# Performance work log

Hardware: AMD Instinct MI355X
Metric: run time of the kernel (lower is better)

Reference implementation:

```python
import jax, jax.numpy as jnp
import numpy as np

N = 100000
E = 1600000
IN_DIM = 256
HID = 256
OUT = 64
K = 10
ALPHA = 0.1


def setup_inputs() -> dict:
    key = jax.random.key(0)
    ks = jax.random.split(key, 8)
    x = jax.random.normal(ks[0], (N, IN_DIM), dtype=jnp.float32)
    edge_index = jax.random.randint(ks[1], (2, E), 0, N, dtype=jnp.int64)
    # Linear params (torch default-ish scale)
    W1 = jax.random.normal(ks[2], (IN_DIM, HID), dtype=jnp.float32) / np.sqrt(IN_DIM)
    b1 = jnp.zeros((HID,), dtype=jnp.float32)
    W2 = jax.random.normal(ks[3], (HID, OUT), dtype=jnp.float32) / np.sqrt(HID)
    b2 = jnp.zeros((OUT,), dtype=jnp.float32)
    alpha = jnp.asarray([ALPHA * (1.0 - ALPHA) ** k for k in range(K + 1)], dtype=jnp.float32)
    return {"x": x, "edge_index": edge_index, "W1": W1, "b1": b1, "W2": W2, "b2": b2, "alpha": alpha}


def reference(x, edge_index, W1, b1, W2, b2, alpha):
    # MLP head (dropout = identity in eval)
    h = jax.nn.relu(x @ W1 + b1) @ W2 + b2  # [N, OUT]

    row, col = edge_index[0], edge_index[1]
    num_nodes = h.shape[0]
    # degree over row (matches torch_geometric degree(row, ...))
    deg = jax.ops.segment_sum(jnp.ones_like(row, dtype=h.dtype), row, num_segments=num_nodes)
    deg_inv_sqrt = jnp.where(deg > 0, jax.lax.rsqrt(jnp.maximum(deg, 1.0)), 0.0)
    norm = deg_inv_sqrt[row] * deg_inv_sqrt[col]  # [E]

    gamma = jax.nn.softmax(alpha)

    def step(carry, g):
        h_cur, acc = carry
        msg = h_cur[col] * norm[:, None]  # gather + scale  [E, OUT]
        h_new = jax.ops.segment_sum(msg, row, num_segments=num_nodes)  # scatter_add
        return (h_new, acc + g * h_new), None

    acc0 = gamma[0] * h
    (_, out), _ = jax.lax.scan(step, (h, acc0), gamma[1:])
    return out
```

## Files before the change

kernel.cpp:

```cpp
#include <hip/hip_runtime.h>
#include <hip/hip_bf16.h>

#define N_NODES 100000
#define N_EDGES 1600000
#define IN_DIM_ 256
#define HID_ 256
#define OUT_ 64
#define KSTEPS 10

typedef __attribute__((ext_vector_type(4))) float f32x4;
typedef __attribute__((ext_vector_type(8))) __bf16 bf16x8;
typedef __attribute__((ext_vector_type(8))) unsigned short u16x8;

static __device__ __forceinline__ unsigned short f2bf(float f) {
    union { float f; unsigned int u; } v; v.f = f;
    unsigned int u = v.u;
    unsigned int r = u + 0x7FFFu + ((u >> 16) & 1u);
    return (unsigned short)(r >> 16);
}
static __device__ __forceinline__ float bflo(unsigned int v) {
    return __uint_as_float(v << 16);
}
static __device__ __forceinline__ float bfhi(unsigned int v) {
    return __uint_as_float(v & 0xFFFF0000u);
}


__global__ void gamma_kernel(const float* __restrict__ alpha, float* __restrict__ gamma) {
    if (threadIdx.x == 0) {
        float m = alpha[0];
        for (int i = 1; i <= KSTEPS; ++i) m = fmaxf(m, alpha[i]);
        float e[KSTEPS + 1];
        float s = 0.f;
        for (int i = 0; i <= KSTEPS; ++i) { e[i] = expf(alpha[i] - m); s += e[i]; }
        float inv = 1.f / s;
        for (int i = 0; i <= KSTEPS; ++i) gamma[i] = e[i] * inv;
    }
}

__global__ void deg_kernel(const int* __restrict__ row, int* __restrict__ deg, int E) {
    int e = blockIdx.x * 256 + threadIdx.x;
    if (e < E) atomicAdd(&deg[row[e]], 1);
}

__global__ void dis_kernel(const int* __restrict__ deg, float* __restrict__ dis, int n) {
    int i = blockIdx.x * 256 + threadIdx.x;
    if (i < n) {
        int d = deg[i];
        dis[i] = d > 0 ? rsqrtf((float)d) : 0.f;
    }
}

__global__ void wcast_kernel(const float* __restrict__ W, unsigned short* __restrict__ wT,
                             int K, int N) {
    int k = blockIdx.x * 256 + threadIdx.x;
    int n = blockIdx.y;
    if (k < K) wT[(size_t)n * K + k] = f2bf(W[(size_t)k * N + n]);
}


__global__ __launch_bounds__(256) void scan_sum_kernel(const int* __restrict__ deg,
                                                       int* __restrict__ bsum, int n) {
    __shared__ int s[256];
    int t = threadIdx.x;
    int i = blockIdx.x * 256 + t;
    s[t] = (i < n) ? deg[i] : 0;
    __syncthreads();
    for (int st = 128; st > 0; st >>= 1) {
        if (t < st) s[t] += s[t + st];
        __syncthreads();
    }
    if (t == 0) bsum[blockIdx.x] = s[0];
}

__global__ __launch_bounds__(512) void scan_block_kernel(int* __restrict__ bsum,
                                                         int* __restrict__ off,
                                                         int nblk, int n) {
    __shared__ int s[512];
    int t = threadIdx.x;
    int v = (t < nblk) ? bsum[t] : 0;
    s[t] = v;
    __syncthreads();
    for (int st = 1; st < 512; st <<= 1) {
        int a = (t >= st) ? s[t - st] : 0;
        __syncthreads();
        s[t] += a;
        __syncthreads();
    }
    if (t < nblk) bsum[t] = s[t] - v;
    if (t == 511) off[n] = s[511];
}

__global__ __launch_bounds__(256) void scan_final_kernel(const int* __restrict__ deg,
                                                         const int* __restrict__ bsum,
                                                         int* __restrict__ off, int n) {
    __shared__ int s[256];
    int t = threadIdx.x;
    int i = blockIdx.x * 256 + t;
    int v = (i < n) ? deg[i] : 0;
    s[t] = v;
    __syncthreads();
    for (int st = 1; st < 256; st <<= 1) {
        int a = (t >= st) ? s[t - st] : 0;
        __syncthreads();
        s[t] += a;
        __syncthreads();
    }
    if (i < n) off[i] = bsum[blockIdx.x] + s[t] - v;
}

__global__ void csr_scatter_kernel(const int* __restrict__ row, const int* __restrict__ col,
                                   const float* __restrict__ dis, const int* __restrict__ off,
                                   int* __restrict__ cursor, int2* __restrict__ ecsr, int E) {
    int e = blockIdx.x * 256 + threadIdx.x;
    if (e < E) {
        int r = row[e], c = col[e];
        float w = dis[r] * dis[c];
        int pos = atomicAdd(&cursor[r], 1);
        int2 p;
        p.x = c;
        p.y = __float_as_int(w);
        ecsr[(size_t)off[r] + pos] = p;
    }
}

__global__ __launch_bounds__(256) void gemm1_kernel(const float* __restrict__ x,
                                                    const unsigned short* __restrict__ w1T,
                                                    const float* __restrict__ b1,
                                                    unsigned short* __restrict__ h1, int M) {
    __shared__ unsigned short As[64][40];
    __shared__ unsigned short Bs[256][40];

    const int tid = threadIdx.x;
    const int lane = tid & 63;
    const int w = tid >> 6;
    const int wr = w >> 1, wc = w & 1;
    const int row0 = blockIdx.x * 64;

    const int am = tid >> 2;
    const int ak = (tid & 3) * 8;

    f32x4 acc[2][8] = {};

    for (int kk = 0; kk < 256; kk += 32) {
        {
            int gr = row0 + am;
            u16x8 av;
            if (gr < M) {
                const float* p = x + (size_t)gr * IN_DIM_ + kk + ak;
                #pragma unroll
                for (int j = 0; j < 8; ++j) av[j] = f2bf(p[j]);
            } else {
                #pragma unroll
                for (int j = 0; j < 8; ++j) av[j] = 0;
            }
            *(u16x8*)&As[am][ak] = av;
        }
        {
            const unsigned short* p = w1T + (size_t)tid * 256 + kk;
            *(u16x8*)&Bs[tid][0]  = *(const u16x8*)&p[0];
            *(u16x8*)&Bs[tid][8]  = *(const u16x8*)&p[8];
            *(u16x8*)&Bs[tid][16] = *(const u16x8*)&p[16];
            *(u16x8*)&Bs[tid][24] = *(const u16x8*)&p[24];
        }
        __syncthreads();

        const int fr = lane & 15;
        const int ko = (lane >> 4) * 8;
        bf16x8 a[2];
        #pragma unroll
        for (int mi = 0; mi < 2; ++mi) a[mi] = *(const bf16x8*)&As[wr * 32 + mi * 16 + fr][ko];
        #pragma unroll
        for (int ni = 0; ni < 8; ++ni) {
            bf16x8 b = *(const bf16x8*)&Bs[wc * 128 + ni * 16 + fr][ko];
            #pragma unroll
            for (int mi = 0; mi < 2; ++mi)
                acc[mi][ni] = __builtin_amdgcn_mfma_f32_16x16x32_bf16(a[mi], b, acc[mi][ni], 0, 0, 0);
        }
        __syncthreads();
    }

    const int fr = lane & 15;
    const int rg = (lane >> 4) * 4;
    #pragma unroll
    for (int mi = 0; mi < 2; ++mi) {
        #pragma unroll
        for (int r = 0; r < 4; ++r) {
            int gm = row0 + wr * 32 + mi * 16 + rg + r;
            if (gm < M) {
                #pragma unroll
                for (int ni = 0; ni < 8; ++ni) {
                    int gn = wc * 128 + ni * 16 + fr;
                    float v = acc[mi][ni][r] + b1[gn];
                    v = fmaxf(v, 0.f);
                    h1[(size_t)gm * HID_ + gn] = f2bf(v);
                }
            }
        }
    }
}

__global__ __launch_bounds__(256) void gemm2_kernel(const unsigned short* __restrict__ h1,
                                                    const unsigned short* __restrict__ w2T,
                                                    const float* __restrict__ b2,
                                                    const float* __restrict__ gamma,
                                                    unsigned short* __restrict__ h,
                                                    float* __restrict__ out, int M) {
    __shared__ unsigned short As[64][40];
    __shared__ unsigned short Bs[64][40];

    const int tid = threadIdx.x;
    const int lane = tid & 63;
    const int w = tid >> 6;
    const int wr = w >> 1, wc = w & 1;
    const int row0 = blockIdx.x * 64;

    const int am = tid >> 2;
    const int ak = (tid & 3) * 8;

    f32x4 acc[2][2] = {};

    for (int kk = 0; kk < 256; kk += 32) {
        {
            int gr = row0 + am;
            if (gr < M) {
                *(u16x8*)&As[am][ak] = *(const u16x8*)&h1[(size_t)gr * HID_ + kk + ak];
            } else {
                u16x8 z = {};
                *(u16x8*)&As[am][ak] = z;
            }
        }
        if (tid < 128) {
            int n = tid >> 1, hf = (tid & 1) * 16;
            const unsigned short* p = &w2T[(size_t)n * 256 + kk + hf];
            *(u16x8*)&Bs[n][hf]     = *(const u16x8*)&p[0];
            *(u16x8*)&Bs[n][hf + 8] = *(const u16x8*)&p[8];
        }
        __syncthreads();

        const int fr = lane & 15;
        const int ko = (lane >> 4) * 8;
        bf16x8 a[2], b[2];
        #pragma unroll
        for (int mi = 0; mi < 2; ++mi) a[mi] = *(const bf16x8*)&As[wr * 32 + mi * 16 + fr][ko];
        #pragma unroll
        for (int ni = 0; ni < 2; ++ni) b[ni] = *(const bf16x8*)&Bs[wc * 32 + ni * 16 + fr][ko];
        #pragma unroll
        for (int mi = 0; mi < 2; ++mi)
            #pragma unroll
            for (int ni = 0; ni < 2; ++ni)
                acc[mi][ni] = __builtin_amdgcn_mfma_f32_16x16x32_bf16(a[mi], b[ni], acc[mi][ni], 0, 0, 0);
        __syncthreads();
    }

    const float g0 = gamma[0];
    const int fr = lane & 15;
    const int rg = (lane >> 4) * 4;
    #pragma unroll
    for (int mi = 0; mi < 2; ++mi) {
        #pragma unroll
        for (int r = 0; r < 4; ++r) {
            int gm = row0 + wr * 32 + mi * 16 + rg + r;
            if (gm < M) {
                #pragma unroll
                for (int ni = 0; ni < 2; ++ni) {
                    int gn = wc * 32 + ni * 16 + fr;
                    float v = acc[mi][ni][r] + b2[gn];
                    h[(size_t)gm * OUT_ + gn] = f2bf(v);
                    out[(size_t)gm * OUT_ + gn] = g0 * v;
                }
            }
        }
    }
}

__global__ __launch_bounds__(256) void pull_kernel(const int* __restrict__ off,
                                                   const int2* __restrict__ ecsr,
                                                   const unsigned short* __restrict__ hc,
                                                   unsigned short* __restrict__ hn,
                                                   float* __restrict__ out,
                                                   const float* __restrict__ gamma,
                                                   int k, int n) {
    int node = blockIdx.x * 4 + (threadIdx.x >> 6);
    if (node >= n) return;
    int lane = threadIdx.x & 63;
    int half = lane >> 5;
    int fl = (lane & 31) * 2;
    int s = off[node], e = off[node + 1];
    float acc0 = 0.f, acc1 = 0.f;

    int j = s + half;
    for (; j + 6 < e; j += 8) {
        int2 pa = ecsr[j];
        int2 pb = ecsr[j + 2];
        int2 pc = ecsr[j + 4];
        int2 pd = ecsr[j + 6];
        unsigned int va = *(const unsigned int*)&hc[(size_t)pa.x * OUT_ + fl];
        unsigned int vb = *(const unsigned int*)&hc[(size_t)pb.x * OUT_ + fl];
        unsigned int vc = *(const unsigned int*)&hc[(size_t)pc.x * OUT_ + fl];
        unsigned int vd = *(const unsigned int*)&hc[(size_t)pd.x * OUT_ + fl];
        float wa = __int_as_float(pa.y), wb = __int_as_float(pb.y);
        float wc = __int_as_float(pc.y), wd = __int_as_float(pd.y);
        acc0 += wa * bflo(va); acc1 += wa * bfhi(va);
        acc0 += wb * bflo(vb); acc1 += wb * bfhi(vb);
        acc0 += wc * bflo(vc); acc1 += wc * bfhi(vc);
        acc0 += wd * bflo(vd); acc1 += wd * bfhi(vd);
    }
    for (; j + 2 < e; j += 4) {
        int2 pa = ecsr[j];
        int2 pb = ecsr[j + 2];
        unsigned int va = *(const unsigned int*)&hc[(size_t)pa.x * OUT_ + fl];
        unsigned int vb = *(const unsigned int*)&hc[(size_t)pb.x * OUT_ + fl];
        float wa = __int_as_float(pa.y), wb = __int_as_float(pb.y);
        acc0 += wa * bflo(va); acc1 += wa * bfhi(va);
        acc0 += wb * bflo(vb); acc1 += wb * bfhi(vb);
    }
    if (j < e) {
        int2 p = ecsr[j];
        unsigned int v = *(const unsigned int*)&hc[(size_t)p.x * OUT_ + fl];
        float w = __int_as_float(p.y);
        acc0 += w * bflo(v);
        acc1 += w * bfhi(v);
    }

    acc0 += __shfl_xor(acc0, 32);
    acc1 += __shfl_xor(acc1, 32);

    if (lane < 32) {
        float g = gamma[k];
        size_t o = (size_t)node * OUT_ + fl;
        unsigned int packed = (unsigned int)f2bf(acc0) | ((unsigned int)f2bf(acc1) << 16);
        *(unsigned int*)&hn[o] = packed;
        float2* op = (float2*)&out[o];
        float2 ov = *op;
        ov.x += g * acc0;
        ov.y += g * acc1;
        *op = ov;
    }
}

extern "C" void kernel_launch(void* const* d_in, const int* in_sizes, int n_in,
                              void* d_out, int out_size, void* d_ws, size_t ws_size,
                              hipStream_t stream) {
    const float* x = (const float*)d_in[0];
    const int* ei = (const int*)d_in[1];
    const float* W1 = (const float*)d_in[2];
    const float* b1 = (const float*)d_in[3];
    const float* W2 = (const float*)d_in[4];
    const float* b2 = (const float*)d_in[5];
    const float* alpha = (const float*)d_in[6];
    const int* row = ei;
    const int* col = ei + N_EDGES;
    float* out = (float*)d_out;

    const int NBLK = (N_NODES + 255) / 256;

    char* wsb = (char*)d_ws;
    size_t p = 0;
    auto alloc = [&](size_t bytes) { size_t r = p; p += (bytes + 255) & ~255ull; return r; };
    float* gamma = (float*)(wsb + alloc(16 * 4));
    int* off     = (int*)(wsb + alloc((N_NODES + 1) * 4));
    int* cursor  = (int*)(wsb + alloc(N_NODES * 4));
    int* deg     = (int*)(wsb + alloc(N_NODES * 4));
    float* dis   = (float*)(wsb + alloc(N_NODES * 4));
    int* bsum    = (int*)(wsb + alloc(512 * 4));
    unsigned short* w1T = (unsigned short*)(wsb + alloc((size_t)IN_DIM_ * HID_ * 2));
    unsigned short* w2T = (unsigned short*)(wsb + alloc((size_t)HID_ * OUT_ * 2));
    int2* ecsr   = (int2*)(wsb + alloc((size_t)N_EDGES * 8));
    unsigned short* h1  = (unsigned short*)(wsb + alloc((size_t)N_NODES * HID_ * 2));
    unsigned short* h_a = (unsigned short*)(wsb + alloc((size_t)N_NODES * OUT_ * 2));
    unsigned short* h_b = h1;

    hipMemsetAsync(cursor, 0, N_NODES * sizeof(int), stream);
    hipMemsetAsync(deg, 0, N_NODES * sizeof(int), stream);
    gamma_kernel<<<1, 64, 0, stream>>>(alpha, gamma);
    deg_kernel<<<(N_EDGES + 255) / 256, 256, 0, stream>>>(row, deg, N_EDGES);
    dis_kernel<<<NBLK, 256, 0, stream>>>(deg, dis, N_NODES);
    scan_sum_kernel<<<NBLK, 256, 0, stream>>>(deg, bsum, N_NODES);
    scan_block_kernel<<<1, 512, 0, stream>>>(bsum, off, NBLK, N_NODES);
    scan_final_kernel<<<NBLK, 256, 0, stream>>>(deg, bsum, off, N_NODES);
    csr_scatter_kernel<<<(N_EDGES + 255) / 256, 256, 0, stream>>>(row, col, dis, off, cursor,
                                                                  ecsr, N_EDGES);
    wcast_kernel<<<dim3(1, HID_), 256, 0, stream>>>(W1, w1T, IN_DIM_, HID_);
    wcast_kernel<<<dim3(1, OUT_), 256, 0, stream>>>(W2, w2T, HID_, OUT_);

    gemm1_kernel<<<(N_NODES + 63) / 64, 256, 0, stream>>>(x, w1T, b1, h1, N_NODES);
    gemm2_kernel<<<(N_NODES + 63) / 64, 256, 0, stream>>>(h1, w2T, b2, gamma, h_a, out, N_NODES);

    unsigned short* hc = h_a;
    unsigned short* hn = h_b;
    for (int k = 1; k <= KSTEPS; ++k) {
        pull_kernel<<<(N_NODES + 3) / 4, 256, 0, stream>>>(off, ecsr, hc, hn, out, gamma, k,
                                                           N_NODES);
        unsigned short* t = hc; hc = hn; hn = t;
    }
}
```

Before: 790.0 us.

## Build CSR via two-pass 64-node bucket scatter and unroll pull loop deeper

Replaces the per-node atomic CSR scatter with two passes. Edges are first appended into 64-node buckets using one global atomic counter per bucket, with the local row index packed into the high bits of the column. A per-bucket kernel then places each edge into its final CSR slot using shared-memory atomics. The goal is to spread atomic traffic over fewer, better-localised counters and make the final writes bucket-local, at the cost of an extra 12.8MB buffer and a second pass. The pull kernel's main loop is also unrolled from 4 to 8 edges per half-wave to keep more gathers in flight.

```diff
diff --git a/kernel.cpp b/kernel.cpp
--- a/kernel.cpp
+++ b/kernel.cpp
@@ -109,18 +109,43 @@
     if (i < n) off[i] = bsum[blockIdx.x] + s[t] - v;
 }
 
-__global__ void csr_scatter_kernel(const int* __restrict__ row, const int* __restrict__ col,
-                                   const float* __restrict__ dis, const int* __restrict__ off,
-                                   int* __restrict__ cursor, int2* __restrict__ ecsr, int E) {
+__global__ void bucket_scatter_kernel(const int* __restrict__ row, const int* __restrict__ col,
+                                      const float* __restrict__ dis, const int* __restrict__ off,
+                                      int* __restrict__ bcur, int2* __restrict__ ebuf, int E) {
     int e = blockIdx.x * 256 + threadIdx.x;
     if (e < E) {
         int r = row[e], c = col[e];
         float w = dis[r] * dis[c];
-        int pos = atomicAdd(&cursor[r], 1);
+        int b = r >> 6;
+        int pos = atomicAdd(&bcur[b], 1);
+        int base = off[b << 6];
         int2 p;
-        p.x = c;
+        p.x = ((r & 63) << 26) | c;
         p.y = __float_as_int(w);
-        ecsr[(size_t)off[r] + pos] = p;
+        ebuf[(size_t)base + pos] = p;
+    }
+}
+
+__global__ __launch_bounds__(256) void bucket_place_kernel(const int* __restrict__ off,
+                                                           const int2* __restrict__ ebuf,
+                                                           int2* __restrict__ ecsr, int n) {
+    __shared__ int cur[64];
+    int b = blockIdx.x;
+    int n0 = b << 6;
+    int nend = min(n0 + 64, n);
+    int t = threadIdx.x;
+    if (t < nend - n0) cur[t] = off[n0 + t];
+    __syncthreads();
+    int lo = off[n0], hi = off[nend];
+    for (int i = lo + t; i < hi; i += 256) {
+        int2 p = ebuf[i];
+        int dlt = (unsigned int)p.x >> 26;
+        int c = p.x & 0x3FFFFFF;
+        int pos = atomicAdd(&cur[dlt], 1);
+        int2 q;
+        q.x = c;
+        q.y = p.y;
+        ecsr[pos] = q;
     }
 }
 
@@ -290,25 +315,32 @@
     float acc0 = 0.f, acc1 = 0.f;
 
     int j = s + half;
-    for (; j + 6 < e; j += 8) {
-        int2 pa = ecsr[j];
-        int2 pb = ecsr[j + 2];
-        int2 pc = ecsr[j + 4];
-        int2 pd = ecsr[j + 6];
-        unsigned int va = *(const unsigned int*)&hc[(size_t)pa.x * OUT_ + fl];
-        unsigned int vb = *(const unsigned int*)&hc[(size_t)pb.x * OUT_ + fl];
-        unsigned int vc = *(const unsigned int*)&hc[(size_t)pc.x * OUT_ + fl];
-        unsigned int vd = *(const unsigned int*)&hc[(size_t)pd.x * OUT_ + fl];
-        float wa = __int_as_float(pa.y), wb = __int_as_float(pb.y);
-        float wc = __int_as_float(pc.y), wd = __int_as_float(pd.y);
-        acc0 += wa * bflo(va); acc1 += wa * bfhi(va);
-        acc0 += wb * bflo(vb); acc1 += wb * bfhi(vb);
-        acc0 += wc * bflo(vc); acc1 += wc * bfhi(vc);
-        acc0 += wd * bflo(vd); acc1 += wd * bfhi(vd);
+    for (; j + 14 < e; j += 16) {
+        int2 p0 = ecsr[j],      p1 = ecsr[j + 2],  p2 = ecsr[j + 4],  p3 = ecsr[j + 6];
+        int2 p4 = ecsr[j + 8],  p5 = ecsr[j + 10], p6 = ecsr[j + 12], p7 = ecsr[j + 14];
+        unsigned int v0 = *(const unsigned int*)&hc[(size_t)p0.x * OUT_ + fl];
+        unsigned int v1 = *(const unsigned int*)&hc[(size_t)p1.x * OUT_ + fl];
+        unsigned int v2 = *(const unsigned int*)&hc[(size_t)p2.x * OUT_ + fl];
+        unsigned int v3 = *(const unsigned int*)&hc[(size_t)p3.x * OUT_ + fl];
+        unsigned int v4 = *(const unsigned int*)&hc[(size_t)p4.x * OUT_ + fl];
+        unsigned int v5 = *(const unsigned int*)&hc[(size_t)p5.x * OUT_ + fl];
+        unsigned int v6 = *(const unsigned int*)&hc[(size_t)p6.x * OUT_ + fl];
+        unsigned int v7 = *(const unsigned int*)&hc[(size_t)p7.x * OUT_ + fl];
+        float w0 = __int_as_float(p0.y), w1 = __int_as_float(p1.y);
+        float w2 = __int_as_float(p2.y), w3 = __int_as_float(p3.y);
+        float w4 = __int_as_float(p4.y), w5 = __int_as_float(p5.y);
+        float w6 = __int_as_float(p6.y), w7 = __int_as_float(p7.y);
+        acc0 += w0 * bflo(v0); acc1 += w0 * bfhi(v0);
+        acc0 += w1 * bflo(v1); acc1 += w1 * bfhi(v1);
+        acc0 += w2 * bflo(v2); acc1 += w2 * bfhi(v2);
+        acc0 += w3 * bflo(v3); acc1 += w3 * bfhi(v3);
+        acc0 += w4 * bflo(v4); acc1 += w4 * bfhi(v4);
+        acc0 += w5 * bflo(v5); acc1 += w5 * bfhi(v5);
+        acc0 += w6 * bflo(v6); acc1 += w6 * bfhi(v6);
+        acc0 += w7 * bflo(v7); acc1 += w7 * bfhi(v7);
     }
     for (; j + 2 < e; j += 4) {
-        int2 pa = ecsr[j];
-        int2 pb = ecsr[j + 2];
+        int2 pa = ecsr[j], pb = ecsr[j + 2];
         unsigned int va = *(const unsigned int*)&hc[(size_t)pa.x * OUT_ + fl];
         unsigned int vb = *(const unsigned int*)&hc[(size_t)pb.x * OUT_ + fl];
         float wa = __int_as_float(pa.y), wb = __int_as_float(pb.y);
@@ -354,24 +386,26 @@
     float* out = (float*)d_out;
 
     const int NBLK = (N_NODES + 255) / 256;
+    const int NBKT = (N_NODES + 63) / 64;
 
     char* wsb = (char*)d_ws;
     size_t p = 0;
     auto alloc = [&](size_t bytes) { size_t r = p; p += (bytes + 255) & ~255ull; return r; };
     float* gamma = (float*)(wsb + alloc(16 * 4));
     int* off     = (int*)(wsb + alloc((N_NODES + 1) * 4));
-    int* cursor  = (int*)(wsb + alloc(N_NODES * 4));
+    int* bcur    = (int*)(wsb + alloc(NBKT * 4));
     int* deg     = (int*)(wsb + alloc(N_NODES * 4));
     float* dis   = (float*)(wsb + alloc(N_NODES * 4));
     int* bsum    = (int*)(wsb + alloc(512 * 4));
     unsigned short* w1T = (unsigned short*)(wsb + alloc((size_t)IN_DIM_ * HID_ * 2));
     unsigned short* w2T = (unsigned short*)(wsb + alloc((size_t)HID_ * OUT_ * 2));
+    int2* ebuf   = (int2*)(wsb + alloc((size_t)N_EDGES * 8));
     int2* ecsr   = (int2*)(wsb + alloc((size_t)N_EDGES * 8));
     unsigned short* h1  = (unsigned short*)(wsb + alloc((size_t)N_NODES * HID_ * 2));
     unsigned short* h_a = (unsigned short*)(wsb + alloc((size_t)N_NODES * OUT_ * 2));
     unsigned short* h_b = h1;
 
-    hipMemsetAsync(cursor, 0, N_NODES * sizeof(int), stream);
+    hipMemsetAsync(bcur, 0, NBKT * sizeof(int), stream);
     hipMemsetAsync(deg, 0, N_NODES * sizeof(int), stream);
     gamma_kernel<<<1, 64, 0, stream>>>(alpha, gamma);
     deg_kernel<<<(N_EDGES + 255) / 256, 256, 0, stream>>>(row, deg, N_EDGES);
@@ -379,8 +413,9 @@
     scan_sum_kernel<<<NBLK, 256, 0, stream>>>(deg, bsum, N_NODES);
     scan_block_kernel<<<1, 512, 0, stream>>>(bsum, off, NBLK, N_NODES);
     scan_final_kernel<<<NBLK, 256, 0, stream>>>(deg, bsum, off, N_NODES);
-    csr_scatter_kernel<<<(N_EDGES + 255) / 256, 256, 0, stream>>>(row, col, dis, off, cursor,
-                                                                  ecsr, N_EDGES);
+    bucket_scatter_kernel<<<(N_EDGES + 255) / 256, 256, 0, stream>>>(row, col, dis, off, bcur,
+                                                                     ebuf, N_EDGES);
+    bucket_place_kernel<<<NBKT, 256, 0, stream>>>(off, ebuf, ecsr, N_NODES);
     wcast_kernel<<<dim3(1, HID_), 256, 0, stream>>>(W1, w1T, IN_DIM_, HID_);
     wcast_kernel<<<dim3(1, OUT_), 256, 0, stream>>>(W2, w2T, HID_, OUT_);
 
```

Measured after the change: 988.0 us. 1.25x slower.

## Slice features into four planes for cache-resident gather; partition CSR scatter

Applied to the files above, without the earlier changes.

Stores h and the output accumulator in four feature-sliced planes of 16 columns each. Each propagation pass then gathers from a 3.2MB bf16 plane, which fits in cache, instead of the full 64-wide table, and a final kernel transposes the output back. The CSR build is split into 8 launches, each handling one row range, so that ecsr writes become more local. The cost is reading the edge list four times per step, extra scatter launches that each re-read row, and narrower 32-byte gathers per neighbour.

```diff
diff --git a/kernel.cpp b/kernel.cpp
--- a/kernel.cpp
+++ b/kernel.cpp
@@ -7,6 +7,8 @@
 #define HID_ 256
 #define OUT_ 64
 #define KSTEPS 10
+#define NSLICE 4
+#define NODEBLK 25000
 
 typedef __attribute__((ext_vector_type(4))) float f32x4;
 typedef __attribute__((ext_vector_type(8))) __bf16 bf16x8;
@@ -111,16 +113,20 @@
 
 __global__ void csr_scatter_kernel(const int* __restrict__ row, const int* __restrict__ col,
                                    const float* __restrict__ dis, const int* __restrict__ off,
-                                   int* __restrict__ cursor, int2* __restrict__ ecsr, int E) {
+                                   int* __restrict__ cursor, int2* __restrict__ ecsr, int E,
+                                   int lo, int hi) {
     int e = blockIdx.x * 256 + threadIdx.x;
     if (e < E) {
-        int r = row[e], c = col[e];
-        float w = dis[r] * dis[c];
-        int pos = atomicAdd(&cursor[r], 1);
-        int2 p;
-        p.x = c;
-        p.y = __float_as_int(w);
-        ecsr[(size_t)off[r] + pos] = p;
+        int r = row[e];
+        if (r >= lo && r < hi) {
+            int c = col[e];
+            float w = dis[r] * dis[c];
+            int pos = atomicAdd(&cursor[r], 1);
+            int2 p;
+            p.x = c;
+            p.y = __float_as_int(w);
+            ecsr[(size_t)off[r] + pos] = p;
+        }
     }
 }
 
@@ -204,8 +210,8 @@
                                                     const unsigned short* __restrict__ w2T,
                                                     const float* __restrict__ b2,
                                                     const float* __restrict__ gamma,
-                                                    unsigned short* __restrict__ h,
-                                                    float* __restrict__ out, int M) {
+                                                    unsigned short* __restrict__ h_t,
+                                                    float* __restrict__ out_t, int M) {
     __shared__ unsigned short As[64][40];
     __shared__ unsigned short Bs[64][40];
 
@@ -266,8 +272,10 @@
                 for (int ni = 0; ni < 2; ++ni) {
                     int gn = wc * 32 + ni * 16 + fr;
                     float v = acc[mi][ni][r] + b2[gn];
-                    h[(size_t)gm * OUT_ + gn] = f2bf(v);
-                    out[(size_t)gm * OUT_ + gn] = g0 * v;
+                    int p = gn >> 4, fo = gn & 15;
+                    size_t o = (size_t)p * M * 16 + (size_t)gm * 16 + fo;
+                    h_t[o] = f2bf(v);
+                    out_t[o] = g0 * v;
                 }
             }
         }
@@ -276,66 +284,65 @@
 
 __global__ __launch_bounds__(256) void pull_kernel(const int* __restrict__ off,
                                                    const int2* __restrict__ ecsr,
-                                                   const unsigned short* __restrict__ hc,
-                                                   unsigned short* __restrict__ hn,
-                                                   float* __restrict__ out,
+                                                   const unsigned short* __restrict__ hc_t,
+                                                   unsigned short* __restrict__ hn_t,
+                                                   float* __restrict__ out_t,
                                                    const float* __restrict__ gamma,
                                                    int k, int n) {
-    int node = blockIdx.x * 4 + (threadIdx.x >> 6);
+    int bid = blockIdx.x;
+    int pass = bid / NODEBLK;
+    int node = (bid % NODEBLK) * 4 + (threadIdx.x >> 6);
     if (node >= n) return;
     int lane = threadIdx.x & 63;
-    int half = lane >> 5;
-    int fl = (lane & 31) * 2;
+    int g = lane >> 3;
+    int fp = lane & 7;
+    const unsigned short* hc = hc_t + (size_t)pass * n * 16;
     int s = off[node], e = off[node + 1];
-    float acc0 = 0.f, acc1 = 0.f;
-
-    int j = s + half;
-    for (; j + 6 < e; j += 8) {
-        int2 pa = ecsr[j];
-        int2 pb = ecsr[j + 2];
-        int2 pc = ecsr[j + 4];
-        int2 pd = ecsr[j + 6];
-        unsigned int va = *(const unsigned int*)&hc[(size_t)pa.x * OUT_ + fl];
-        unsigned int vb = *(const unsigned int*)&hc[(size_t)pb.x * OUT_ + fl];
-        unsigned int vc = *(const unsigned int*)&hc[(size_t)pc.x * OUT_ + fl];
-        unsigned int vd = *(const unsigned int*)&hc[(size_t)pd.x * OUT_ + fl];
-        float wa = __int_as_float(pa.y), wb = __int_as_float(pb.y);
-        float wc = __int_as_float(pc.y), wd = __int_as_float(pd.y);
-        acc0 += wa * bflo(va); acc1 += wa * bfhi(va);
-        acc0 += wb * bflo(vb); acc1 += wb * bfhi(vb);
-        acc0 += wc * bflo(vc); acc1 += wc * bfhi(vc);
-        acc0 += wd * bflo(vd); acc1 += wd * bfhi(vd);
-    }
-    for (; j + 2 < e; j += 4) {
-        int2 pa = ecsr[j];
-        int2 pb = ecsr[j + 2];
-        unsigned int va = *(const unsigned int*)&hc[(size_t)pa.x * OUT_ + fl];
-        unsigned int vb = *(const unsigned int*)&hc[(size_t)pb.x * OUT_ + fl];
-        float wa = __int_as_float(pa.y), wb = __int_as_float(pb.y);
-        acc0 += wa * bflo(va); acc1 += wa * bfhi(va);
-        acc0 += wb * bflo(vb); acc1 += wb * bfhi(vb);
+    float a0 = 0.f, a1 = 0.f;
+
+    int j = s + g;
+    for (; j + 8 < e; j += 16) {
+        int2 pA = ecsr[j];
+        int2 pB = ecsr[j + 8];
+        unsigned int vA = *(const unsigned int*)&hc[(size_t)pA.x * 16 + fp * 2];
+        unsigned int vB = *(const unsigned int*)&hc[(size_t)pB.x * 16 + fp * 2];
+        float wA = __int_as_float(pA.y), wB = __int_as_float(pB.y);
+        a0 += wA * bflo(vA); a1 += wA * bfhi(vA);
+        a0 += wB * bflo(vB); a1 += wB * bfhi(vB);
     }
     if (j < e) {
         int2 p = ecsr[j];
-        unsigned int v = *(const unsigned int*)&hc[(size_t)p.x * OUT_ + fl];
+        unsigned int v = *(const unsigned int*)&hc[(size_t)p.x * 16 + fp * 2];
         float w = __int_as_float(p.y);
-        acc0 += w * bflo(v);
-        acc1 += w * bfhi(v);
-    }
-
-    acc0 += __shfl_xor(acc0, 32);
-    acc1 += __shfl_xor(acc1, 32);
-
-    if (lane < 32) {
-        float g = gamma[k];
-        size_t o = (size_t)node * OUT_ + fl;
-        unsigned int packed = (unsigned int)f2bf(acc0) | ((unsigned int)f2bf(acc1) << 16);
-        *(unsigned int*)&hn[o] = packed;
-        float2* op = (float2*)&out[o];
+        a0 += w * bflo(v);
+        a1 += w * bfhi(v);
+    }
+
+    a0 += __shfl_xor(a0, 8);  a1 += __shfl_xor(a1, 8);
+    a0 += __shfl_xor(a0, 16); a1 += __shfl_xor(a1, 16);
+    a0 += __shfl_xor(a0, 32); a1 += __shfl_xor(a1, 32);
+
+    if (lane < 8) {
+        float gk = gamma[k];
+        size_t o = (size_t)pass * n * 16 + (size_t)node * 16 + fp * 2;
+        unsigned int packed = (unsigned int)f2bf(a0) | ((unsigned int)f2bf(a1) << 16);
+        *(unsigned int*)&hn_t[o] = packed;
+        float2* op = (float2*)&out_t[o];
         float2 ov = *op;
-        ov.x += g * acc0;
-        ov.y += g * acc1;
+        ov.x += gk * a0;
+        ov.y += gk * a1;
         *op = ov;
+    }
+}
+
+__global__ __launch_bounds__(256) void detrans_kernel(const float* __restrict__ out_t,
+                                                      float* __restrict__ out, int n) {
+    int i = blockIdx.x * 256 + threadIdx.x;
+    if (i < n * 16) {
+        int node = i >> 4, f4 = i & 15;
+        int p = f4 >> 2, q = f4 & 3;
+        f32x4 v = *(const f32x4*)&out_t[(size_t)p * n * 16 + (size_t)node * 16 + q * 4];
+        *(f32x4*)&out[(size_t)node * 64 + f4 * 4] = v;
     }
 }
 
@@ -367,6 +374,7 @@
     unsigned short* w1T = (unsigned short*)(wsb + alloc((size_t)IN_DIM_ * HID_ * 2));
     unsigned short* w2T = (unsigned short*)(wsb + alloc((size_t)HID_ * OUT_ * 2));
     int2* ecsr   = (int2*)(wsb + alloc((size_t)N_EDGES * 8));
+    float* out_t = (float*)(wsb + alloc((size_t)N_NODES * OUT_ * 4));
     unsigned short* h1  = (unsigned short*)(wsb + alloc((size_t)N_NODES * HID_ * 2));
     unsigned short* h_a = (unsigned short*)(wsb + alloc((size_t)N_NODES * OUT_ * 2));
     unsigned short* h_b = h1;
@@ -379,19 +387,23 @@
     scan_sum_kernel<<<NBLK, 256, 0, stream>>>(deg, bsum, N_NODES);
     scan_block_kernel<<<1, 512, 0, stream>>>(bsum, off, NBLK, N_NODES);
     scan_final_kernel<<<NBLK, 256, 0, stream>>>(deg, bsum, off, N_NODES);
-    csr_scatter_kernel<<<(N_EDGES + 255) / 256, 256, 0, stream>>>(row, col, dis, off, cursor,
-                                                                  ecsr, N_EDGES);
+    for (int s = 0; s < 8; ++s) {
+        csr_scatter_kernel<<<(N_EDGES + 255) / 256, 256, 0, stream>>>(
+            row, col, dis, off, cursor, ecsr, N_EDGES, s * 12500, (s + 1) * 12500);
+    }
     wcast_kernel<<<dim3(1, HID_), 256, 0, stream>>>(W1, w1T, IN_DIM_, HID_);
     wcast_kernel<<<dim3(1, OUT_), 256, 0, stream>>>(W2, w2T, HID_, OUT_);
 
     gemm1_kernel<<<(N_NODES + 63) / 64, 256, 0, stream>>>(x, w1T, b1, h1, N_NODES);
-    gemm2_kernel<<<(N_NODES + 63) / 64, 256, 0, stream>>>(h1, w2T, b2, gamma, h_a, out, N_NODES);
+    gemm2_kernel<<<(N_NODES + 63) / 64, 256, 0, stream>>>(h1, w2T, b2, gamma, h_a, out_t,
+                                                          N_NODES);
 
     unsigned short* hc = h_a;
     unsigned short* hn = h_b;
     for (int k = 1; k <= KSTEPS; ++k) {
-        pull_kernel<<<(N_NODES + 3) / 4, 256, 0, stream>>>(off, ecsr, hc, hn, out, gamma, k,
-                                                           N_NODES);
+        pull_kernel<<<NODEBLK * NSLICE, 256, 0, stream>>>(off, ecsr, hc, hn, out_t, gamma, k,
+                                                          N_NODES);
         unsigned short* t = hc; hc = hn; hn = t;
     }
-}
+    detrans_kernel<<<(N_NODES * 16 + 255) / 256, 256, 0, stream>>>(out_t, out, N_NODES);
+}
```

Measured after the change: 1.533 ms. 1.94x slower.
